# Performance work log

Hardware: AMD Instinct MI355X
Metric: run time of the kernel (lower is better)

The kernel has to match this reference:

```python
import jax, jax.numpy as jnp
import numpy as np

NUM_EDGE = 5
NUM_CHANNELS = 2
NUM_NODES = 2048
W_IN = 256
W_OUT = 128
NUM_CLASS = 16
NUM_LAYERS = 2


def gtconv(A, w):
    """Softmax-weighted mix of edge-type adjacencies.
    A: [E, N, N], w: [E, C] -> [C, N, N].
    Equivalent to concatenating COO edge lists scaled by filter[j, i] and
    summing duplicates (what the scipy round-trip does implicitly)."""
    f = jax.nn.softmax(w, axis=0)  # softmax over edge types (dim=0)
    return jnp.einsum('enm,ec->cnm', A, f)


def degree_normalize(H):
    """GTN.normalization: deg = scatter_add over col, value *= deg[col]^-1 (col scaling).
    H: [C, N, N]; deg over rows (axis=1) gives per-column in-degree."""
    deg = H.sum(axis=1)  # [C, N]
    dinv = jnp.where(deg > 0, 1.0 / jnp.where(deg > 0, deg, 1.0), 0.0)
    return H * dinv[:, None, :]


def setup_inputs() -> dict:
    key = jax.random.key(0)
    ks = jax.random.split(key, 8)
    A = jax.random.uniform(ks[0], (NUM_EDGE, NUM_NODES, NUM_NODES), dtype=jnp.float32)
    h = jax.random.normal(ks[1], (NUM_NODES, W_IN), dtype=jnp.float32)
    # GTConv weights: init std=0.01 as in reset_parameters
    w1 = jax.random.normal(ks[2], (NUM_EDGE, NUM_CHANNELS), dtype=jnp.float32) * 0.01
    w2 = jax.random.normal(ks[3], (NUM_EDGE, NUM_CHANNELS), dtype=jnp.float32) * 0.01
    w_layers = jax.random.normal(ks[4], (NUM_LAYERS - 1, NUM_EDGE, NUM_CHANNELS), dtype=jnp.float32) * 0.01
    gcn_w = jax.random.normal(ks[5], (W_IN, W_OUT), dtype=jnp.float32) * (1.0 / np.sqrt(W_IN))
    gcn_b = jnp.zeros((W_OUT,), dtype=jnp.float32)
    lin1_w = jax.random.normal(ks[6], (W_OUT * NUM_CHANNELS, W_OUT), dtype=jnp.float32) * (1.0 / np.sqrt(W_OUT * NUM_CHANNELS))
    lin1_b = jnp.zeros((W_OUT,), dtype=jnp.float32)
    lin2_w = jax.random.normal(ks[7], (W_OUT, NUM_CLASS), dtype=jnp.float32) * (1.0 / np.sqrt(W_OUT))
    lin2_b = jnp.zeros((NUM_CLASS,), dtype=jnp.float32)
    return {"A": A, "h": h, "w1": w1, "w2": w2, "w_layers": w_layers,
            "gcn_w": gcn_w, "gcn_b": gcn_b, "lin1_w": lin1_w, "lin1_b": lin1_b,
            "lin2_w": lin2_w, "lin2_b": lin2_b}


def reference(A, h, w1, w2, w_layers, gcn_w, gcn_b, lin1_w, lin1_b, lin2_w, lin2_b):
    # Layer 0 (first=True): H[c] = conv1(A)[c] @ conv2(A)[c], then degree norm.
    H = jnp.einsum('cnk,ckm->cnm', gtconv(A, w1), gtconv(A, w2))
    H = degree_normalize(H)
    # Layers 1..L-1 (first=False): H[c] = H[c] @ conv(A)[c], then degree norm.
    for i in range(w_layers.shape[0]):
        B = gtconv(A, w_layers[i])
        H = jnp.einsum('cnk,ckm->cnm', H, B)
        H = degree_normalize(H)
    # Shared GCN per channel (DGL GraphConv, norm='both'): weight first (w_in > w_out),
    # src out-degree^-1/2 scaling, aggregate along edges src->dst, dst in-degree^-1/2.
    hw = h @ gcn_w                                   # [N, w_out]
    dout = jnp.clip(H.sum(axis=2), 1.0, None) ** -0.5  # [C, N] src norm
    din = jnp.clip(H.sum(axis=1), 1.0, None) ** -0.5   # [C, N] dst norm
    agg = jnp.einsum('cnm,cnd->cmd', H, dout[:, :, None] * hw[None])  # dst m gathers from src n
    X = jax.nn.relu(agg * din[:, :, None] + gcn_b)   # [C, N, w_out]
    # Concatenate channels along feature dim (channel-major, matching th.cat order)
    X = jnp.transpose(X, (1, 0, 2)).reshape(H.shape[1], -1)  # [N, C*w_out]
    X = jax.nn.relu(X @ lin1_w + lin1_b)
    return X @ lin2_w + lin2_b
```

## Files before the change

kernel.cpp:

```cpp
#include <hip/hip_runtime.h>

typedef unsigned short u16;
typedef __attribute__((ext_vector_type(4))) float f32x4;
typedef __attribute__((ext_vector_type(8))) __bf16 bf16x8;
typedef __attribute__((ext_vector_type(8))) unsigned short us8;

#define NN (2048ull*2048ull)

__device__ __forceinline__ u16 f2b(float x){
  union { float f; unsigned u; } v; v.f = x;
  unsigned r = v.u + 0x7FFFu + ((v.u >> 16) & 1u);
  return (u16)(r >> 16);
}
__device__ __forceinline__ float b2f(u16 x){
  union { unsigned u; float f; } v; v.u = ((unsigned)x) << 16; return v.f;
}

__global__ __launch_bounds__(256)
void k_mix(const float* __restrict__ A,
           const float* __restrict__ w1, const float* __restrict__ w2,
           const float* __restrict__ wl,
           u16* __restrict__ A1T, u16* __restrict__ A2T, u16* __restrict__ BT,
           float* __restrict__ sA1, float* __restrict__ deg2){
  __shared__ u16 lt[2][64][68];
  const int t = threadIdx.x;
  const int mq = t & 15, nr = t >> 4;
  const int n0 = blockIdx.y * 64, m0 = blockIdx.x * 64;
  float f[3][2][5];
  #pragma unroll
  for (int s=0;s<3;s++){
    const float* w = (s==0) ? w1 : (s==1) ? w2 : wl;
    #pragma unroll
    for (int c=0;c<2;c++){
      float m = -1e30f;
      #pragma unroll
      for (int e=0;e<5;e++) m = fmaxf(m, w[e*2+c]);
      float sum = 0.f;
      #pragma unroll
      for (int e=0;e<5;e++){ f[s][c][e] = __expf(w[e*2+c]-m); sum += f[s][c][e]; }
      float inv = 1.f/sum;
      #pragma unroll
      for (int e=0;e<5;e++) f[s][c][e] *= inv;
    }
  }

  ushort4 reg[6][4];
  #pragma unroll
  for (int rr=0; rr<4; ++rr){
    const int nl = nr*4 + rr;
    const size_t off = (size_t)(n0+nl)*2048 + m0 + mq*4;
    float4 a0 = *(const float4*)&A[off];
    float4 a1 = *(const float4*)&A[NN + off];
    float4 a2 = *(const float4*)&A[2*NN + off];
    float4 a3 = *(const float4*)&A[3*NN + off];
    float4 a4 = *(const float4*)&A[4*NN + off];
    float ax[4][5] = {{a0.x,a1.x,a2.x,a3.x,a4.x},
                      {a0.y,a1.y,a2.y,a3.y,a4.y},
                      {a0.z,a1.z,a2.z,a3.z,a4.z},
                      {a0.w,a1.w,a2.w,a3.w,a4.w}};
    #pragma unroll
    for (int c=0;c<2;c++){
      #pragma unroll
      for (int j=0;j<4;j++){
        float s1=0.f,s2=0.f,s3=0.f;
        #pragma unroll
        for (int e=0;e<5;e++){
          s1 += ax[j][e]*f[0][c][e];
          s2 += ax[j][e]*f[1][c][e];
          s3 += ax[j][e]*f[2][c][e];
        }
        ((u16*)&reg[0+c][rr])[j] = f2b(s1);
        ((u16*)&reg[2+c][rr])[j] = f2b(s2);
        ((u16*)&reg[4+c][rr])[j] = f2b(s3);
      }
    }
  }

  const int nq = t & 15, mr = t >> 4;
  for (int s=0; s<3; ++s){
    if (s) __syncthreads();
    #pragma unroll
    for (int c=0;c<2;c++){
      #pragma unroll
      for (int j=0;j<4;j++){
        ushort4 o;
        o.x = ((const u16*)&reg[s*2+c][0])[j];
        o.y = ((const u16*)&reg[s*2+c][1])[j];
        o.z = ((const u16*)&reg[s*2+c][2])[j];
        o.w = ((const u16*)&reg[s*2+c][3])[j];
        *(ushort4*)&lt[c][mq*4+j][nr*4] = o;
      }
    }
    __syncthreads();
    u16* __restrict__ dst = (s==0) ? A1T : (s==1) ? A2T : BT;
    #pragma unroll
    for (int c=0;c<2;c++){
      #pragma unroll
      for (int rr=0;rr<4;rr++){
        const int ml = mr*4 + rr;
        ushort4 o = *(const ushort4*)&lt[c][ml][nq*4];
        *(ushort4*)&dst[(size_t)c*NN + (size_t)(m0+ml)*2048 + n0 + nq*4] = o;
        if (s != 1){
          float part = b2f(o.x)+b2f(o.y)+b2f(o.z)+b2f(o.w);
          part += __shfl_xor(part, 1); part += __shfl_xor(part, 2);
          part += __shfl_xor(part, 4); part += __shfl_xor(part, 8);
          if (nq == 0){
            float* tgt = (s==0) ? sA1 : deg2;
            atomicAdd(&tgt[c*2048 + m0 + ml], part);
          }
        }
      }
    }
  }
}

__global__ __launch_bounds__(256)
void k_deg1(const u16* __restrict__ A2T, const float* __restrict__ sA1,
            float* __restrict__ deg1){
  const int g = blockIdx.x*4 + (threadIdx.x >> 6);
  const int lane = threadIdx.x & 63;
  const int c = g >> 11, j = g & 2047;
  const u16* __restrict__ row = A2T + (size_t)c*NN + (size_t)j*2048;
  const float* __restrict__ sv = sA1 + c*2048;
  float s = 0.f;
  #pragma unroll
  for (int it=0; it<4; ++it){
    const int k = it*512 + lane*8;
    us8 v = *(const us8*)&row[k];
    const float4 f0 = *(const float4*)&sv[k];
    const float4 f1 = *(const float4*)&sv[k+4];
    s += b2f(v[0])*f0.x + b2f(v[1])*f0.y + b2f(v[2])*f0.z + b2f(v[3])*f0.w
       + b2f(v[4])*f1.x + b2f(v[5])*f1.y + b2f(v[6])*f1.z + b2f(v[7])*f1.w;
  }
  s += __shfl_xor(s, 1);  s += __shfl_xor(s, 2);  s += __shfl_xor(s, 4);
  s += __shfl_xor(s, 8);  s += __shfl_xor(s, 16); s += __shfl_xor(s, 32);
  if (lane == 0) deg1[c*2048 + j] = s;
}

template<int MODE>
__global__ __launch_bounds__(256)
void k_wsum(const u16* __restrict__ MT, const float* __restrict__ va,
            const float* __restrict__ vb, float* __restrict__ outv){
  __shared__ float w[64];
  const int t = threadIdx.x;
  const int n = blockIdx.x * 256 + t;
  const int m0 = blockIdx.y * 64;
  const int c = blockIdx.z;
  if (t < 64){
    const int m = c*2048 + m0 + t;
    float x;
    if (MODE == 0){ float d = va[m]; x = d > 0.f ? 1.f/d : 0.f; }
    else if (MODE == 1){ float d = va[m]; x = (d > 0.f ? 1.f/d : 0.f) * vb[m]; }
    else { x = va[m]; }
    w[t] = x;
  }
  __syncthreads();
  const u16* __restrict__ p = MT + (size_t)c*NN + (size_t)m0*2048 + n;
  float s = 0.f;
  #pragma unroll 4
  for (int m=0;m<64;m++)
    s += b2f(p[(size_t)m*2048]) * w[m];
  atomicAdd(&outv[c*2048 + n], s);
}

__global__ __launch_bounds__(256)
void k_hwpt(const float* __restrict__ h, const float* __restrict__ W,
            const float* __restrict__ rowsum, u16* __restrict__ PT){
  __shared__ float lh[8][256];
  int t = threadIdx.x;
  int n0 = blockIdx.x * 8;
  for (int idx = t; idx < 8*256; idx += 256)
    lh[idx >> 8][idx & 255] = h[(size_t)(n0 + (idx>>8))*256 + (idx&255)];
  __syncthreads();
  int d = t & 127, half = t >> 7;
  float acc[4];
  #pragma unroll
  for (int nn=0;nn<4;nn++) acc[nn] = 0.f;
  for (int k=0;k<256;k++){
    float wv = W[(size_t)k*128 + d];
    #pragma unroll
    for (int nn=0;nn<4;nn++) acc[nn] += lh[half*4+nn][k]*wv;
  }
  #pragma unroll
  for (int c=0;c<2;c++){
    ushort4 o;
    #pragma unroll
    for (int nn=0;nn<4;nn++){
      int n = n0 + half*4 + nn;
      float dv = rsqrtf(fmaxf(rowsum[c*2048 + n], 1.0f));
      ((u16*)&o)[nn] = f2b(dv * acc[nn]);
    }
    *(ushort4*)&PT[((size_t)c*128 + d)*2048 + n0 + half*4] = o;
  }
}

__global__ __launch_bounds__(256, 2)
void k_gemm3(const u16* __restrict__ A, const u16* __restrict__ Bt, float* __restrict__ Agg){
  __shared__ u16 lA[128*64];
  __shared__ u16 lB[128*64];
  const int tid = threadIdx.x;
  const int bm = blockIdx.x, bk = blockIdx.y, cc = blockIdx.z;
  const u16* __restrict__ Ab = A + (size_t)cc*NN + (size_t)(bm*128)*2048 + bk*256;
  const u16* __restrict__ Bb = Bt + (size_t)cc*(128*2048) + bk*256;
  float* __restrict__ Cb = Agg + (size_t)cc*2048*128 + (size_t)(bm*128)*128;
  const int wid = tid >> 6, lane = tid & 63;
  const int wr = wid >> 1, wc = wid & 1;
  const int fl = lane & 15, fk = (lane >> 4) << 3;
  const int srow = (wid << 3) + (lane >> 3);
  const int scol = (lane & 7) << 3;

  f32x4 acc[4][4];
  const f32x4 zero = {0.f,0.f,0.f,0.f};
  #pragma unroll
  for (int i=0;i<4;i++)
    #pragma unroll
    for (int jj=0;jj<4;jj++) acc[i][jj] = zero;

  for (int k0 = 0; k0 < 256; k0 += 64){
    #pragma unroll
    for (int it = 0; it < 4; ++it){
      int r = it*32 + srow;
      __builtin_amdgcn_global_load_lds(
        (const __attribute__((address_space(1))) void*)(Ab + (size_t)r*2048 + k0 + scol),
        (__attribute__((address_space(3))) void*)(&lA[(it*32 + (wid<<3))*64]), 16, 0, 0);
      __builtin_amdgcn_global_load_lds(
        (const __attribute__((address_space(1))) void*)(Bb + (size_t)r*2048 + k0 + scol),
        (__attribute__((address_space(3))) void*)(&lB[(it*32 + (wid<<3))*64]), 16, 0, 0);
    }
    __syncthreads();
    #pragma unroll
    for (int ks = 0; ks < 2; ++ks){
      bf16x8 af[4], bfr[4];
      #pragma unroll
      for (int mi=0;mi<4;mi++)
        af[mi] = *reinterpret_cast<const bf16x8*>(&lA[(wr*64 + mi*16 + fl)*64 + ks*32 + fk]);
      #pragma unroll
      for (int ni=0;ni<4;ni++)
        bfr[ni] = *reinterpret_cast<const bf16x8*>(&lB[(wc*64 + ni*16 + fl)*64 + ks*32 + fk]);
      #pragma unroll
      for (int mi=0;mi<4;mi++)
        #pragma unroll
        for (int ni=0;ni<4;ni++)
          acc[mi][ni] = __builtin_amdgcn_mfma_f32_16x16x32_bf16(af[mi], bfr[ni], acc[mi][ni], 0, 0, 0);
    }
    __syncthreads();
  }
  const int rbase = (lane >> 4) << 2;
  #pragma unroll
  for (int mi=0;mi<4;mi++)
    #pragma unroll
    for (int ni=0;ni<4;ni++)
      #pragma unroll
      for (int r=0;r<4;r++)
        atomicAdd(&Cb[(size_t)(wr*64 + mi*16 + rbase + r)*128 + wc*64 + ni*16 + fl],
                  acc[mi][ni][r]);
}

template<bool SCALE>
__global__ __launch_bounds__(256)
void k_qt(const float* __restrict__ Agg, const float* __restrict__ deg1,
          u16* __restrict__ QT){
  __shared__ u16 lq[128][36];
  const int t = threadIdx.x;
  const int m0 = blockIdx.x * 32, c = blockIdx.y;
  const int d4 = (t & 31) * 4, mr = t >> 5;
  #pragma unroll
  for (int p4=0; p4<4; ++p4){
    const int m = m0 + p4*8 + mr;
    float4 s = *(const float4*)&Agg[((size_t)c*2048 + m)*128 + d4];
    if (SCALE){
      float dg = deg1[c*2048 + m];
      float di = dg > 0.f ? 1.f/dg : 0.f;
      s.x *= di; s.y *= di; s.z *= di; s.w *= di;
    }
    const int ml = p4*8 + mr;
    lq[d4+0][ml] = f2b(s.x); lq[d4+1][ml] = f2b(s.y);
    lq[d4+2][ml] = f2b(s.z); lq[d4+3][ml] = f2b(s.w);
  }
  __syncthreads();
  const int d = t >> 1, half = t & 1;
  u16* __restrict__ dst = QT + ((size_t)c*128 + d)*2048 + m0 + half*16;
  #pragma unroll
  for (int q=0;q<4;q++){
    ushort4 o;
    o.x = lq[d][half*16 + q*4 + 0];
    o.y = lq[d][half*16 + q*4 + 1];
    o.z = lq[d][half*16 + q*4 + 2];
    o.w = lq[d][half*16 + q*4 + 3];
    *(ushort4*)&dst[q*4] = o;
  }
}

__global__ __launch_bounds__(256)
void k_head(const float* __restrict__ agg3, const float* __restrict__ deg2,
            const float* __restrict__ gb,
            const float* __restrict__ W1, const float* __restrict__ b1,
            const float* __restrict__ W2, const float* __restrict__ b2,
            float* __restrict__ out){
  __shared__ float lx[8][256];
  __shared__ float lt[8][132];
  int t = threadIdx.x;
  int n0 = blockIdx.x * 8;
  for (int idx = t; idx < 512; idx += 256){
    int row = idx >> 6;
    int q = idx & 63;
    int c = q >> 5, d4 = (q & 31) * 4;
    float dg = deg2[c*2048 + n0 + row];
    float di = dg > 0.f ? 1.f/dg : 0.f;
    float4 s = *(const float4*)&agg3[((size_t)c*2048 + n0 + row)*128 + d4];
    const float4 bv = *(const float4*)&gb[d4];
    s.x = fmaxf(s.x*di + bv.x, 0.f); s.y = fmaxf(s.y*di + bv.y, 0.f);
    s.z = fmaxf(s.z*di + bv.z, 0.f); s.w = fmaxf(s.w*di + bv.w, 0.f);
    *(float4*)&lx[row][c*128 + d4] = s;
  }
  __syncthreads();
  int d = t & 127, half = t >> 7;
  float acc[4];
  #pragma unroll
  for (int nn=0;nn<4;nn++) acc[nn] = 0.f;
  for (int k=0;k<256;k++){
    float wv = W1[(size_t)k*128 + d];
    #pragma unroll
    for (int nn=0;nn<4;nn++) acc[nn] += lx[half*4+nn][k]*wv;
  }
  float bb = b1[d];
  #pragma unroll
  for (int nn=0;nn<4;nn++){
    float v = acc[nn] + bb;
    lt[half*4+nn][d] = v > 0.f ? v : 0.f;
  }
  __syncthreads();
  if (t < 128){
    int row = t >> 4, q = t & 15;
    float s = b2[q];
    for (int dd=0; dd<128; dd++) s += lt[row][dd] * W2[(size_t)dd*16 + q];
    out[(size_t)(n0+row)*16 + q] = s;
  }
}

extern "C" void kernel_launch(void* const* d_in, const int* in_sizes, int n_in,
                              void* d_out, int out_size, void* d_ws, size_t ws_size,
                              hipStream_t stream){
  const float* A   = (const float*)d_in[0];
  const float* h   = (const float*)d_in[1];
  const float* w1  = (const float*)d_in[2];
  const float* w2  = (const float*)d_in[3];
  const float* wl  = (const float*)d_in[4];
  const float* gw  = (const float*)d_in[5];
  const float* gb  = (const float*)d_in[6];
  const float* l1w = (const float*)d_in[7];
  const float* l1b = (const float*)d_in[8];
  const float* l2w = (const float*)d_in[9];
  const float* l2b = (const float*)d_in[10];
  float* out = (float*)d_out;
  char* ws = (char*)d_ws;

  const size_t SZ = 2*NN*2;
  const size_t AGG = (size_t)2*2048*128*4;
  u16*  A1T  = (u16*)(ws);
  u16*  A2T  = (u16*)(ws + 1*SZ);
  u16*  BT   = (u16*)(ws + 2*SZ);
  char* tail = ws + 3*SZ;
  u16*  PT     = (u16*)tail;
  u16*  Q1T    = (u16*)(tail + 1048576);
  u16*  Q2T    = (u16*)(tail + 2*1048576);
  float* sA1   = (float*)(tail + 3*1048576);
  float* deg1  = sA1 + 4096;
  float* deg2  = deg1 + 4096;
  float* v1    = deg2 + 4096;
  float* v3    = v1 + 4096;
  float* rowsum= v3 + 4096;
  float* agg1  = rowsum + 4096;
  float* agg2  = agg1 + 2*2048*128;
  float* agg3  = agg2 + 2*2048*128;
  const size_t ZBYTES = 6*4096*4 + 3*AGG;

  const size_t TOTAL = 3*SZ + 3*1048576 + ZBYTES;
  if (ws_size < TOTAL){ hipMemsetAsync(d_out, 0, (size_t)out_size*4, stream); return; }

  hipMemsetAsync(sA1, 0, ZBYTES, stream);

  k_mix<<<dim3(32,32), 256, 0, stream>>>(A, w1, w2, wl, A1T, A2T, BT, sA1, deg2);
  k_deg1<<<1024, 256, 0, stream>>>(A2T, sA1, deg1);
  k_wsum<0><<<dim3(8,32,2), 256, 0, stream>>>(BT, deg2, deg2, v1);
  k_wsum<1><<<dim3(8,32,2), 256, 0, stream>>>(A2T, deg1, v1, v3);
  k_wsum<2><<<dim3(8,32,2), 256, 0, stream>>>(A1T, v3, v3, rowsum);
  k_hwpt<<<256, 256, 0, stream>>>(h, gw, rowsum, PT);
  k_gemm3<<<dim3(16,8,2), 256, 0, stream>>>(A1T, PT, agg1);
  k_qt<false><<<dim3(64,2), 256, 0, stream>>>(agg1, deg1, Q1T);
  k_gemm3<<<dim3(16,8,2), 256, 0, stream>>>(A2T, Q1T, agg2);
  k_qt<true><<<dim3(64,2), 256, 0, stream>>>(agg2, deg1, Q2T);
  k_gemm3<<<dim3(16,8,2), 256, 0, stream>>>(BT, Q2T, agg3);
  k_head<<<256, 256, 0, stream>>>(agg3, deg2, gb, l1w, l1b, l2w, l2b, out);
}
```

Before: 160.0 us.

## Store mixed adjacencies in tiled blocked layout instead of transposing through LDS

The mixing kernel now loads A through global_load_lds into a staging buffer and writes each mixed adjacency in a 16x256 blocked tile layout, with no transpose through shared memory. The degree and weighted-sum kernels are rewritten to read this layout, and the first GEMM computes blocked addresses for its A operand. The memset is replaced by a small zeroing kernel. This targets the transpose and shuffle overhead in the dominant memory-bound mixing pass, but the GEMM's A loads now stride across tiles, which may hurt their coalescing.

```diff
diff --git a/kernel.cpp b/kernel.cpp
--- a/kernel.cpp
+++ b/kernel.cpp
@@ -7,6 +7,7 @@
 
 #define NN (2048ull*2048ull)
 
+
 __device__ __forceinline__ u16 f2b(float x){
   union { float f; unsigned u; } v; v.f = x;
   unsigned r = v.u + 0x7FFFu + ((v.u >> 16) & 1u);
@@ -14,6 +15,13 @@
 }
 __device__ __forceinline__ float b2f(u16 x){
   union { unsigned u; float f; } v; v.u = ((unsigned)x) << 16; return v.f;
+}
+
+__global__ __launch_bounds__(256)
+void k_zero(float4* __restrict__ p, int n4){
+  const float4 z = {0.f,0.f,0.f,0.f};
+  for (int i = blockIdx.x*256 + threadIdx.x; i < n4; i += gridDim.x*256)
+    p[i] = z;
 }
 
 __global__ __launch_bounds__(256)
@@ -22,10 +30,12 @@
            const float* __restrict__ wl,
            u16* __restrict__ A1T, u16* __restrict__ A2T, u16* __restrict__ BT,
            float* __restrict__ sA1, float* __restrict__ deg2){
-  __shared__ u16 lt[2][64][68];
+  __shared__ float stg[16*256];
   const int t = threadIdx.x;
-  const int mq = t & 15, nr = t >> 4;
-  const int n0 = blockIdx.y * 64, m0 = blockIdx.x * 64;
+  const int mt = blockIdx.x;
+  const int nt = blockIdx.y;
+  const int m0 = mt*256, n0 = nt*16;
+
   float f[3][2][5];
   #pragma unroll
   for (int s=0;s<3;s++){
@@ -44,123 +54,118 @@
     }
   }
 
-  ushort4 reg[6][4];
-  #pragma unroll
-  for (int rr=0; rr<4; ++rr){
-    const int nl = nr*4 + rr;
-    const size_t off = (size_t)(n0+nl)*2048 + m0 + mq*4;
-    float4 a0 = *(const float4*)&A[off];
-    float4 a1 = *(const float4*)&A[NN + off];
-    float4 a2 = *(const float4*)&A[2*NN + off];
-    float4 a3 = *(const float4*)&A[3*NN + off];
-    float4 a4 = *(const float4*)&A[4*NN + off];
-    float ax[4][5] = {{a0.x,a1.x,a2.x,a3.x,a4.x},
-                      {a0.y,a1.y,a2.y,a3.y,a4.y},
-                      {a0.z,a1.z,a2.z,a3.z,a4.z},
-                      {a0.w,a1.w,a2.w,a3.w,a4.w}};
-    #pragma unroll
-    for (int c=0;c<2;c++){
-      #pragma unroll
-      for (int j=0;j<4;j++){
-        float s1=0.f,s2=0.f,s3=0.f;
+  float acc[6][16];
+  #pragma unroll
+  for (int sc=0;sc<6;sc++)
+    #pragma unroll
+    for (int n=0;n<16;n++) acc[sc][n] = 0.f;
+
+  #pragma unroll
+  for (int e=0;e<5;e++){
+    #pragma unroll
+    for (int it=0; it<4; ++it)
+      __builtin_amdgcn_global_load_lds(
+        (const __attribute__((address_space(1))) void*)
+          (A + (size_t)e*NN + (size_t)(n0 + it*4 + (t>>6))*2048 + m0 + (t&63)*4),
+        (__attribute__((address_space(3))) void*)(&stg[it*1024 + t*4]), 16, 0, 0);
+    __syncthreads();
+    #pragma unroll
+    for (int n=0;n<16;n++){
+      float a = stg[n*256 + t];
+      #pragma unroll
+      for (int s=0;s<3;s++)
         #pragma unroll
-        for (int e=0;e<5;e++){
-          s1 += ax[j][e]*f[0][c][e];
-          s2 += ax[j][e]*f[1][c][e];
-          s3 += ax[j][e]*f[2][c][e];
-        }
-        ((u16*)&reg[0+c][rr])[j] = f2b(s1);
-        ((u16*)&reg[2+c][rr])[j] = f2b(s2);
-        ((u16*)&reg[4+c][rr])[j] = f2b(s3);
-      }
-    }
-  }
-
-  const int nq = t & 15, mr = t >> 4;
-  for (int s=0; s<3; ++s){
-    if (s) __syncthreads();
-    #pragma unroll
-    for (int c=0;c<2;c++){
-      #pragma unroll
-      for (int j=0;j<4;j++){
-        ushort4 o;
-        o.x = ((const u16*)&reg[s*2+c][0])[j];
-        o.y = ((const u16*)&reg[s*2+c][1])[j];
-        o.z = ((const u16*)&reg[s*2+c][2])[j];
-        o.w = ((const u16*)&reg[s*2+c][3])[j];
-        *(ushort4*)&lt[c][mq*4+j][nr*4] = o;
-      }
+        for (int c=0;c<2;c++)
+          acc[s*2+c][n] += a * f[s][c][e];
     }
     __syncthreads();
-    u16* __restrict__ dst = (s==0) ? A1T : (s==1) ? A2T : BT;
-    #pragma unroll
-    for (int c=0;c<2;c++){
-      #pragma unroll
-      for (int rr=0;rr<4;rr++){
-        const int ml = mr*4 + rr;
-        ushort4 o = *(const ushort4*)&lt[c][ml][nq*4];
-        *(ushort4*)&dst[(size_t)c*NN + (size_t)(m0+ml)*2048 + n0 + nq*4] = o;
-        if (s != 1){
-          float part = b2f(o.x)+b2f(o.y)+b2f(o.z)+b2f(o.w);
-          part += __shfl_xor(part, 1); part += __shfl_xor(part, 2);
-          part += __shfl_xor(part, 4); part += __shfl_xor(part, 8);
-          if (nq == 0){
-            float* tgt = (s==0) ? sA1 : deg2;
-            atomicAdd(&tgt[c*2048 + m0 + ml], part);
-          }
-        }
-      }
-    }
-  }
-}
-
-__global__ __launch_bounds__(256)
-void k_deg1(const u16* __restrict__ A2T, const float* __restrict__ sA1,
+  }
+
+  #pragma unroll
+  for (int c=0;c<2;c++){
+    float p1 = 0.f, pB = 0.f;
+    #pragma unroll
+    for (int n=0;n<16;n++){ p1 += acc[0+c][n]; pB += acc[4+c][n]; }
+    atomicAdd(&sA1[c*2048 + m0 + t], p1);
+    atomicAdd(&deg2[c*2048 + m0 + t], pB);
+  }
+  const size_t tb = (size_t)(nt*8 + mt)*4096 + (size_t)t*16;
+  #pragma unroll
+  for (int sc=0; sc<6; ++sc){
+    u16* __restrict__ dst = (sc<2) ? A1T : (sc<4) ? A2T : BT;
+    const int c = sc & 1;
+    us8 v0, v1;
+    #pragma unroll
+    for (int q=0;q<8;q++){ v0[q] = f2b(acc[sc][q]); v1[q] = f2b(acc[sc][8+q]); }
+    *(us8*)&dst[(size_t)c*NN + tb]     = v0;
+    *(us8*)&dst[(size_t)c*NN + tb + 8] = v1;
+  }
+}
+
+__global__ __launch_bounds__(256)
+void k_rdot(const u16* __restrict__ A2T, const float* __restrict__ sA1,
             float* __restrict__ deg1){
-  const int g = blockIdx.x*4 + (threadIdx.x >> 6);
-  const int lane = threadIdx.x & 63;
-  const int c = g >> 11, j = g & 2047;
-  const u16* __restrict__ row = A2T + (size_t)c*NN + (size_t)j*2048;
+  const int mt = blockIdx.x, ng = blockIdx.y, c = blockIdx.z;
+  const int t = threadIdx.x;
+  const u16* __restrict__ Mc = A2T + (size_t)c*NN;
   const float* __restrict__ sv = sA1 + c*2048;
   float s = 0.f;
-  #pragma unroll
-  for (int it=0; it<4; ++it){
-    const int k = it*512 + lane*8;
-    us8 v = *(const us8*)&row[k];
-    const float4 f0 = *(const float4*)&sv[k];
-    const float4 f1 = *(const float4*)&sv[k+4];
-    s += b2f(v[0])*f0.x + b2f(v[1])*f0.y + b2f(v[2])*f0.z + b2f(v[3])*f0.w
-       + b2f(v[4])*f1.x + b2f(v[5])*f1.y + b2f(v[6])*f1.z + b2f(v[7])*f1.w;
-  }
-  s += __shfl_xor(s, 1);  s += __shfl_xor(s, 2);  s += __shfl_xor(s, 4);
-  s += __shfl_xor(s, 8);  s += __shfl_xor(s, 16); s += __shfl_xor(s, 32);
-  if (lane == 0) deg1[c*2048 + j] = s;
+  #pragma unroll 2
+  for (int q=0; q<16; ++q){
+    const int ntile = ng*16 + q;
+    const u16* base = Mc + (size_t)(ntile*8 + mt)*4096 + (size_t)t*16;
+    us8 v0 = *(const us8*)base;
+    us8 v1 = *(const us8*)(base + 8);
+    const float4 f0 = *(const float4*)&sv[ntile*16 + 0];
+    const float4 f1 = *(const float4*)&sv[ntile*16 + 4];
+    const float4 f2 = *(const float4*)&sv[ntile*16 + 8];
+    const float4 f3 = *(const float4*)&sv[ntile*16 + 12];
+    s += b2f(v0[0])*f0.x + b2f(v0[1])*f0.y + b2f(v0[2])*f0.z + b2f(v0[3])*f0.w
+       + b2f(v0[4])*f1.x + b2f(v0[5])*f1.y + b2f(v0[6])*f1.z + b2f(v0[7])*f1.w
+       + b2f(v1[0])*f2.x + b2f(v1[1])*f2.y + b2f(v1[2])*f2.z + b2f(v1[3])*f2.w
+       + b2f(v1[4])*f3.x + b2f(v1[5])*f3.y + b2f(v1[6])*f3.z + b2f(v1[7])*f3.w;
+  }
+  atomicAdd(&deg1[c*2048 + mt*256 + t], s);
 }
 
 template<int MODE>
 __global__ __launch_bounds__(256)
 void k_wsum(const u16* __restrict__ MT, const float* __restrict__ va,
             const float* __restrict__ vb, float* __restrict__ outv){
-  __shared__ float w[64];
+  __shared__ float w[512];
+  __shared__ float red[16][17];
   const int t = threadIdx.x;
-  const int n = blockIdx.x * 256 + t;
-  const int m0 = blockIdx.y * 64;
-  const int c = blockIdx.z;
-  if (t < 64){
-    const int m = c*2048 + m0 + t;
+  const int nt = blockIdx.x, mgrp = blockIdx.y, c = blockIdx.z;
+  #pragma unroll
+  for (int i=t; i<512; i+=256){
+    const int m = c*2048 + mgrp*512 + i;
     float x;
     if (MODE == 0){ float d = va[m]; x = d > 0.f ? 1.f/d : 0.f; }
     else if (MODE == 1){ float d = va[m]; x = (d > 0.f ? 1.f/d : 0.f) * vb[m]; }
     else { x = va[m]; }
-    w[t] = x;
-  }
-  __syncthreads();
-  const u16* __restrict__ p = MT + (size_t)c*NN + (size_t)m0*2048 + n;
+    w[i] = x;
+  }
+  __syncthreads();
+  const int n = t & 15, mg = t >> 4;
   float s = 0.f;
-  #pragma unroll 4
-  for (int m=0;m<64;m++)
-    s += b2f(p[(size_t)m*2048]) * w[m];
-  atomicAdd(&outv[c*2048 + n], s);
+  #pragma unroll
+  for (int mt2=0; mt2<2; ++mt2){
+    const u16* __restrict__ base = MT + (size_t)c*NN
+        + (size_t)(nt*8 + mgrp*2 + mt2)*4096 + n;
+    #pragma unroll 4
+    for (int mm=0; mm<16; ++mm){
+      const int ml = mg*16 + mm;
+      s += b2f(base[ml*16]) * w[mt2*256 + ml];
+    }
+  }
+  red[mg][n] = s;
+  __syncthreads();
+  if (t < 16){
+    float sum = 0.f;
+    #pragma unroll
+    for (int g=0; g<16; ++g) sum += red[g][t];
+    atomicAdd(&outv[c*2048 + nt*16 + t], sum);
+  }
 }
 
 __global__ __launch_bounds__(256)
@@ -200,7 +205,6 @@
   __shared__ u16 lB[128*64];
   const int tid = threadIdx.x;
   const int bm = blockIdx.x, bk = blockIdx.y, cc = blockIdx.z;
-  const u16* __restrict__ Ab = A + (size_t)cc*NN + (size_t)(bm*128)*2048 + bk*256;
   const u16* __restrict__ Bb = Bt + (size_t)cc*(128*2048) + bk*256;
   float* __restrict__ Cb = Agg + (size_t)cc*2048*128 + (size_t)(bm*128)*128;
   const int wid = tid >> 6, lane = tid & 63;
@@ -219,10 +223,14 @@
   for (int k0 = 0; k0 < 256; k0 += 64){
     #pragma unroll
     for (int it = 0; it < 4; ++it){
+      const int m = bm*128 + it*32 + srow;
+      const int n = bk*256 + k0 + scol;
+      const u16* srcA = A + (size_t)cc*NN
+          + (size_t)((n>>4)*8 + (m>>8))*4096 + (size_t)(m&255)*16 + (n&15);
+      __builtin_amdgcn_global_load_lds(
+        (const __attribute__((address_space(1))) void*)srcA,
+        (__attribute__((address_space(3))) void*)(&lA[(it*32 + (wid<<3))*64]), 16, 0, 0);
       int r = it*32 + srow;
-      __builtin_amdgcn_global_load_lds(
-        (const __attribute__((address_space(1))) void*)(Ab + (size_t)r*2048 + k0 + scol),
-        (__attribute__((address_space(3))) void*)(&lA[(it*32 + (wid<<3))*64]), 16, 0, 0);
       __builtin_amdgcn_global_load_lds(
         (const __attribute__((address_space(1))) void*)(Bb + (size_t)r*2048 + k0 + scol),
         (__attribute__((address_space(3))) void*)(&lB[(it*32 + (wid<<3))*64]), 16, 0, 0);
@@ -378,13 +386,13 @@
   const size_t TOTAL = 3*SZ + 3*1048576 + ZBYTES;
   if (ws_size < TOTAL){ hipMemsetAsync(d_out, 0, (size_t)out_size*4, stream); return; }
 
-  hipMemsetAsync(sA1, 0, ZBYTES, stream);
-
-  k_mix<<<dim3(32,32), 256, 0, stream>>>(A, w1, w2, wl, A1T, A2T, BT, sA1, deg2);
-  k_deg1<<<1024, 256, 0, stream>>>(A2T, sA1, deg1);
-  k_wsum<0><<<dim3(8,32,2), 256, 0, stream>>>(BT, deg2, deg2, v1);
-  k_wsum<1><<<dim3(8,32,2), 256, 0, stream>>>(A2T, deg1, v1, v3);
-  k_wsum<2><<<dim3(8,32,2), 256, 0, stream>>>(A1T, v3, v3, rowsum);
+  k_zero<<<1024, 256, 0, stream>>>((float4*)sA1, (int)(ZBYTES/16));
+
+  k_mix<<<dim3(8,128), 256, 0, stream>>>(A, w1, w2, wl, A1T, A2T, BT, sA1, deg2);
+  k_rdot<<<dim3(8,8,2), 256, 0, stream>>>(A2T, sA1, deg1);
+  k_wsum<0><<<dim3(128,4,2), 256, 0, stream>>>(BT, deg2, deg2, v1);
+  k_wsum<1><<<dim3(128,4,2), 256, 0, stream>>>(A2T, deg1, v1, v3);
+  k_wsum<2><<<dim3(128,4,2), 256, 0, stream>>>(A1T, v3, v3, rowsum);
   k_hwpt<<<256, 256, 0, stream>>>(h, gw, rowsum, PT);
   k_gemm3<<<dim3(16,8,2), 256, 0, stream>>>(A1T, PT, agg1);
   k_qt<false><<<dim3(64,2), 256, 0, stream>>>(agg1, deg1, Q1T);
```

New measurement: 149.6 us. -6.5%, faster.
